# Performance work log

Hardware: AMD Instinct MI355X
Metric: run time of the kernel (lower is better)

The kernel has to match this reference:

```python
import jax, jax.numpy as jnp
import numpy as np

HEADS = 16
DIM_HEAD = 64
SCALE = DIM_HEAD ** -0.5


def setup_inputs() -> dict:
    key = jax.random.key(0)
    ks = jax.random.split(key, 5)
    b, n, dim = 2, 2048, 1024
    inner = HEADS * DIM_HEAD  # 1024
    std = dim ** -0.5
    return {
        "x": jax.random.normal(ks[0], (b, n, dim), jnp.float32),
        "ln_gamma": jnp.ones((dim,), jnp.float32),
        "ln_beta": jnp.zeros((dim,), jnp.float32),
        "W_qk": jax.random.normal(ks[1], (dim, 2 * inner), jnp.float32) * std,
        "W_v": jax.random.normal(ks[2], (dim, inner), jnp.float32) * std,
        "W_out": jax.random.normal(ks[3], (inner, dim), jnp.float32) * std,
        "b_out": jnp.zeros((dim,), jnp.float32),
    }


def _layernorm(x, gamma, beta, eps=1e-5):
    mu = jnp.mean(x, axis=-1, keepdims=True)
    var = jnp.var(x, axis=-1, keepdims=True)
    return (x - mu) * jax.lax.rsqrt(var + eps) * gamma + beta


def reference(x, ln_gamma, ln_beta, W_qk, W_v, W_out, b_out):
    b, n, dim = x.shape
    h, d = HEADS, DIM_HEAD
    xn = _layernorm(x, ln_gamma, ln_beta)
    qk = xn @ W_qk                      # [b, n, 2*h*d]
    q, k = jnp.split(qk, 2, axis=-1)    # each [b, n, h*d]
    v = xn @ W_v                        # [b, n, h*d]
    # b n (h d) -> b h n d
    q = q.reshape(b, n, h, d).transpose(0, 2, 1, 3)
    k = k.reshape(b, n, h, d).transpose(0, 2, 1, 3)
    v = v.reshape(b, n, h, d).transpose(0, 2, 1, 3)
    dots = jnp.einsum('bhid,bhjd->bhij', q, k) * SCALE
    attn = jax.nn.softmax(dots, axis=-1)
    out = jnp.einsum('bhij,bhjd->bhid', attn, v)
    out = out.transpose(0, 2, 1, 3).reshape(b, n, h * d)
    return out @ W_out + b_out
```

## Files before the change

### kernel.cpp

```cpp
#include <hip/hip_runtime.h>

#define HEADS 16
#define DHEAD 64
#define BATCH 2
#define SEQ   2048
#define DIM   1024
#define ROWS  (BATCH*SEQ)
#define SCALE_LOG2E 0.180336880f

typedef short v8s __attribute__((ext_vector_type(8)));
typedef float v4f __attribute__((ext_vector_type(4)));

__device__ __forceinline__ float fast_exp2(float x) {
    return __builtin_amdgcn_exp2f(x);
}

__device__ __forceinline__ unsigned short f2bf(float f) {
    unsigned u = __float_as_uint(f);
    u += 0x7FFFu + ((u >> 16) & 1u);
    return (unsigned short)(u >> 16);
}

__device__ __forceinline__ unsigned pk_bf2(float hi, float lo) {
    return __builtin_amdgcn_perm(__float_as_uint(hi), __float_as_uint(lo), 0x07060302u);
}

#define GLDS16(g, l) __builtin_amdgcn_global_load_lds( \
    (__attribute__((address_space(1))) void*)(g), \
    (__attribute__((address_space(3))) void*)(l), 16, 0, 0)

__global__ __launch_bounds__(256) void ln_kernel(const float* __restrict__ x,
                                                 const float* __restrict__ gamma,
                                                 const float* __restrict__ beta,
                                                 unsigned short* __restrict__ xn) {
    int row = blockIdx.x;
    const float* xr = x + (size_t)row * DIM;
    int t = threadIdx.x;
    float4 v = *(const float4*)(xr + t * 4);
    float s  = v.x + v.y + v.z + v.w;
    float sq = v.x * v.x + v.y * v.y + v.z * v.z + v.w * v.w;
#pragma unroll
    for (int off = 32; off > 0; off >>= 1) {
        s  += __shfl_down(s,  off, 64);
        sq += __shfl_down(sq, off, 64);
    }
    __shared__ float ss[4], ssq[4];
    int wave = t >> 6, lane = t & 63;
    if (lane == 0) { ss[wave] = s; ssq[wave] = sq; }
    __syncthreads();
    float tot  = ss[0] + ss[1] + ss[2] + ss[3];
    float totq = ssq[0] + ssq[1] + ssq[2] + ssq[3];
    float mean = tot * (1.f / DIM);
    float var  = totq * (1.f / DIM) - mean * mean;
    float rstd = rsqrtf(var + 1e-5f);
    float4 g = *(const float4*)(gamma + t * 4);
    float4 bb = *(const float4*)(beta + t * 4);
    ushort4 o;
    o.x = f2bf((v.x - mean) * rstd * g.x + bb.x);
    o.y = f2bf((v.y - mean) * rstd * g.y + bb.y);
    o.z = f2bf((v.z - mean) * rstd * g.z + bb.z);
    o.w = f2bf((v.w - mean) * rstd * g.w + bb.w);
    *(ushort4*)(xn + (size_t)row * DIM + t * 4) = o;
}

__global__ __launch_bounds__(256) void tr_all_kernel(const float* __restrict__ Wqk,
                                                     const float* __restrict__ Wv,
                                                     const float* __restrict__ Wout,
                                                     unsigned short* __restrict__ Tqk,
                                                     unsigned short* __restrict__ Tv,
                                                     unsigned short* __restrict__ To) {
    int z = blockIdx.z;
    const float* W = (z == 0) ? Wqk : (z == 1) ? Wv : Wout;
    unsigned short* Wt = (z == 0) ? Tqk : (z == 1) ? Tv : To;
    int Nw = (z == 0) ? 2048 : 1024;
    int n0 = blockIdx.x * 64, k0 = blockIdx.y * 64;
    if (n0 >= Nw) return;
    __shared__ float tile[64][65];
    int tid = threadIdx.x;
#pragma unroll
    for (int l = 0; l < 4; ++l) {
        int kk = (tid >> 4) + l * 16;
        int nn = (tid & 15) * 4;
        float4 v = *(const float4*)(W + (size_t)(k0 + kk) * Nw + n0 + nn);
        tile[kk][nn + 0] = v.x; tile[kk][nn + 1] = v.y;
        tile[kk][nn + 2] = v.z; tile[kk][nn + 3] = v.w;
    }
    __syncthreads();
#pragma unroll
    for (int l = 0; l < 4; ++l) {
        int cid = tid + l * 256;
        int nn = cid >> 4, kc = (cid & 15) * 4;
        ushort4 o;
        o.x = f2bf(tile[kc + 0][nn]);
        o.y = f2bf(tile[kc + 1][nn]);
        o.z = f2bf(tile[kc + 2][nn]);
        o.w = f2bf(tile[kc + 3][nn]);
        *(ushort4*)(Wt + (size_t)(n0 + nn) * DIM + k0 + kc) = o;
    }
}

template<int BN, bool SWAP>
__device__ __forceinline__ void mm_core2(const unsigned short* __restrict__ A,
                                         const unsigned short* __restrict__ Bt,
                                         int K, int aTile, int bTile,
                                         unsigned short (*As)[32],
                                         unsigned short (*Bs)[32],
                                         v4f (*acc)[4]) {
    constexpr int MI = (BN == 128) ? 4 : 2;
    int t = threadIdx.x;
    int w = t >> 6, L = t & 63, l15 = L & 15, quad = L >> 4;
    int aOff = (BN == 128) ? (w >> 1) * 64 : w * 32;
    int bOff = (BN == 128) ? (w & 1) * 64 : 0;
    int srow = L >> 2, schunk = (L & 3) * 8;
    for (int k0 = 0; k0 < K; k0 += 32) {
        __syncthreads();
#pragma unroll
        for (int j = 0; j < 2; ++j) {
            int g = w * 2 + j;
            GLDS16(A + (size_t)(aTile + g * 16 + srow) * K + k0 + schunk,
                   &As[g * 16][0]);
        }
#pragma unroll
        for (int j = 0; j < BN / 64; ++j) {
            int g = (BN == 128) ? (w * 2 + j) : w;
            GLDS16(Bt + (size_t)(bTile + g * 16 + srow) * K + k0 + schunk,
                   &Bs[g * 16][0]);
        }
        __syncthreads();
        v8s a[MI], b[4];
#pragma unroll
        for (int i = 0; i < MI; ++i) a[i] = *(const v8s*)&As[aOff + i * 16 + l15][quad * 8];
#pragma unroll
        for (int j = 0; j < 4; ++j) b[j] = *(const v8s*)&Bs[bOff + j * 16 + l15][quad * 8];
#pragma unroll
        for (int i = 0; i < MI; ++i)
#pragma unroll
            for (int j = 0; j < 4; ++j)
                acc[i][j] = SWAP
                    ? __builtin_amdgcn_mfma_f32_16x16x32_bf16(b[j], a[i], acc[i][j], 0, 0, 0)
                    : __builtin_amdgcn_mfma_f32_16x16x32_bf16(a[i], b[j], acc[i][j], 0, 0, 0);
    }
}

__global__ __launch_bounds__(256) void gemm_qkv_kernel(const unsigned short* __restrict__ A,
                                                       const unsigned short* __restrict__ Bt,
                                                       unsigned short* __restrict__ q_h,
                                                       unsigned short* __restrict__ k_h,
                                                       unsigned short* __restrict__ v_t) {
    __shared__ __align__(16) unsigned short As[128][32];
    __shared__ __align__(16) unsigned short Bs[128][32];
    int t = threadIdx.x, w = t >> 6, L = t & 63, l15 = L & 15, quad = L >> 4;
    int aTile = blockIdx.y * 128, bTile = blockIdx.x * 128;
    int aOff = (w >> 1) * 64, bOff = (w & 1) * 64;
    v4f acc[4][4] = {};
    if (bTile < 2048) {
        mm_core2<128, true>(A, Bt, DIM, aTile, bTile, As, Bs, acc);
        float sc = (bTile < 1024) ? SCALE_LOG2E : 1.0f;
#pragma unroll
        for (int j = 0; j < 4; ++j) {
            int col = bTile + bOff + j * 16 + quad * 4;
            unsigned short* dst = (col < 1024) ? q_h : k_h;
            int c = col & 1023;
            int h = c >> 6, d = c & 63;
#pragma unroll
            for (int i = 0; i < 4; ++i) {
                int m = aTile + aOff + i * 16 + l15;
                int b = m >> 11, seq = m & 2047;
                ushort4 o;
                o.x = f2bf(acc[i][j][0] * sc); o.y = f2bf(acc[i][j][1] * sc);
                o.z = f2bf(acc[i][j][2] * sc); o.w = f2bf(acc[i][j][3] * sc);
                *(ushort4*)(dst + (((size_t)(b * 16 + h)) * SEQ + seq) * 64 + d) = o;
            }
        }
    } else {
        mm_core2<128, false>(A, Bt, DIM, aTile, bTile, As, Bs, acc);
#pragma unroll
        for (int j = 0; j < 4; ++j) {
            int c = bTile + bOff + j * 16 + l15 - 2048;
            int h = c >> 6, d = c & 63;
#pragma unroll
            for (int i = 0; i < 4; ++i) {
                int m0 = aTile + aOff + i * 16 + quad * 4;
                int b = m0 >> 11, seq0 = m0 & 2047;
                ushort4 o;
                o.x = f2bf(acc[i][j][0]); o.y = f2bf(acc[i][j][1]);
                o.z = f2bf(acc[i][j][2]); o.w = f2bf(acc[i][j][3]);
                *(ushort4*)(v_t + (((size_t)(b * 16 + h)) * 64 + d) * SEQ + seq0) = o;
            }
        }
    }
}

__global__ __launch_bounds__(256) void gemm_out_kernel(const unsigned short* __restrict__ A,
                                                       const unsigned short* __restrict__ Bt,
                                                       const float* __restrict__ bias,
                                                       float* __restrict__ C) {
    __shared__ __align__(16) unsigned short As[128][32];
    __shared__ __align__(16) unsigned short Bs[64][32];
    int t = threadIdx.x, w = t >> 6, L = t & 63, l15 = L & 15, quad = L >> 4;
    int aTile = blockIdx.y * 128, bTile = blockIdx.x * 64;
    v4f acc[2][4] = {};
    mm_core2<64, true>(A, Bt, DIM, aTile, bTile, As, Bs, acc);
#pragma unroll
    for (int j = 0; j < 4; ++j) {
        int n = bTile + j * 16 + quad * 4;
        float4 bv = *(const float4*)(bias + n);
#pragma unroll
        for (int i = 0; i < 2; ++i) {
            int m = aTile + w * 32 + i * 16 + l15;
            float4 o = make_float4(acc[i][j][0] + bv.x, acc[i][j][1] + bv.y,
                                   acc[i][j][2] + bv.z, acc[i][j][3] + bv.w);
            *(float4*)(C + (size_t)m * DIM + n) = o;
        }
    }
}

__global__ __launch_bounds__(256) void attn_kernel(const unsigned short* __restrict__ q_h,
                                                   const unsigned short* __restrict__ k_h,
                                                   const unsigned short* __restrict__ v_t,
                                                   unsigned short* __restrict__ ao) {
    __shared__ __align__(16) unsigned short KF[2][8 * 64 * 8];
    __shared__ __align__(16) unsigned short VF[2][8 * 64 * 8];
    __shared__ __align__(16) unsigned short Pld[4][2][16 * 72];
    int bid = blockIdx.x;
    int wg = (bid & 7) * 64 + (bid >> 3);
    int qt = wg & 15, h = (wg >> 4) & 15, b = wg >> 8;
    int bh = b * HEADS + h;
    int w = threadIdx.x >> 6;
    int L = threadIdx.x & 63, l15 = L & 15, quad = L >> 4;

    const unsigned short* qp = q_h + ((size_t)bh * SEQ + qt * 128 + w * 32 + l15) * 64 + quad * 8;
    v8s qf[2][2];
    qf[0][0] = *(const v8s*)(qp);
    qf[0][1] = *(const v8s*)(qp + 32);
    qf[1][0] = *(const v8s*)(qp + 16 * 64);
    qf[1][1] = *(const v8s*)(qp + 16 * 64 + 32);

    const unsigned short* ksrc = k_h + ((size_t)bh * SEQ + w * 16 + l15) * 64 + quad * 8;
    const unsigned short* vsrc = v_t + ((size_t)bh * 64 + w * 16 + l15) * SEQ + quad * 8;

    GLDS16(ksrc,      &KF[0][(w * 2 + 0) * 512]);
    GLDS16(ksrc + 32, &KF[0][(w * 2 + 1) * 512]);
    GLDS16(vsrc,      &VF[0][(w * 2 + 0) * 512]);
    GLDS16(vsrc + 32, &VF[0][(w * 2 + 1) * 512]);

    v4f o[2][4] = {};
    v4f lacc[2] = {};
    const short ob = (short)0x3F80;
    const v8s ones = {ob, ob, ob, ob, ob, ob, ob, ob};

    int cur = 0;
    for (int j0 = 0; j0 < SEQ; j0 += 64) {
        __syncthreads();
        if (j0 + 64 < SEQ) {
            const unsigned short* kn = ksrc + (size_t)(j0 + 64) * 64;
            const unsigned short* vn = vsrc + (j0 + 64);
            GLDS16(kn,      &KF[cur ^ 1][(w * 2 + 0) * 512]);
            GLDS16(kn + 32, &KF[cur ^ 1][(w * 2 + 1) * 512]);
            GLDS16(vn,      &VF[cur ^ 1][(w * 2 + 0) * 512]);
            GLDS16(vn + 32, &VF[cur ^ 1][(w * 2 + 1) * 512]);
        }
        v8s kf[4][2], vf[4][2];
#pragma unroll
        for (int jt = 0; jt < 4; ++jt) {
            kf[jt][0] = *(const v8s*)&KF[cur][((jt * 2 + 0) * 64 + L) * 8];
            kf[jt][1] = *(const v8s*)&KF[cur][((jt * 2 + 1) * 64 + L) * 8];
            vf[jt][0] = *(const v8s*)&VF[cur][((jt * 2 + 0) * 64 + L) * 8];
            vf[jt][1] = *(const v8s*)&VF[cur][((jt * 2 + 1) * 64 + L) * 8];
        }
        v4f s[2][4] = {};
        __builtin_amdgcn_s_setprio(1);
#pragma unroll
        for (int m = 0; m < 2; ++m)
#pragma unroll
            for (int jt = 0; jt < 4; ++jt) {
                s[m][jt] = __builtin_amdgcn_mfma_f32_16x16x32_bf16(kf[jt][0], qf[m][0], s[m][jt], 0, 0, 0);
                s[m][jt] = __builtin_amdgcn_mfma_f32_16x16x32_bf16(kf[jt][1], qf[m][1], s[m][jt], 0, 0, 0);
            }
        __builtin_amdgcn_s_setprio(0);
#pragma unroll
        for (int m = 0; m < 2; ++m)
#pragma unroll
            for (int jt = 0; jt < 4; ++jt) {
                float p0 = fast_exp2(s[m][jt][0]);
                float p1 = fast_exp2(s[m][jt][1]);
                float p2 = fast_exp2(s[m][jt][2]);
                float p3 = fast_exp2(s[m][jt][3]);
                uint2 pk;
                pk.x = pk_bf2(p1, p0);
                pk.y = pk_bf2(p3, p2);
                *(uint2*)&Pld[w][m][l15 * 72 + jt * 16 + quad * 4] = pk;
            }
#pragma unroll
        for (int m = 0; m < 2; ++m) {
            v8s pb0 = *(const v8s*)&Pld[w][m][l15 * 72 + quad * 8];
            v8s pb1 = *(const v8s*)&Pld[w][m][l15 * 72 + 32 + quad * 8];
            __builtin_amdgcn_s_setprio(1);
#pragma unroll
            for (int dt = 0; dt < 4; ++dt) {
                o[m][dt] = __builtin_amdgcn_mfma_f32_16x16x32_bf16(vf[dt][0], pb0, o[m][dt], 0, 0, 0);
                o[m][dt] = __builtin_amdgcn_mfma_f32_16x16x32_bf16(vf[dt][1], pb1, o[m][dt], 0, 0, 0);
            }
            lacc[m] = __builtin_amdgcn_mfma_f32_16x16x32_bf16(ones, pb0, lacc[m], 0, 0, 0);
            lacc[m] = __builtin_amdgcn_mfma_f32_16x16x32_bf16(ones, pb1, lacc[m], 0, 0, 0);
            __builtin_amdgcn_s_setprio(0);
        }
        cur ^= 1;
    }
#pragma unroll
    for (int m = 0; m < 2; ++m) {
        float inv = 1.f / lacc[m][0];
        int rowg = b * SEQ + qt * 128 + w * 32 + m * 16 + l15;
#pragma unroll
        for (int dt = 0; dt < 4; ++dt) {
            ushort4 ov;
            ov.x = f2bf(o[m][dt][0] * inv);
            ov.y = f2bf(o[m][dt][1] * inv);
            ov.z = f2bf(o[m][dt][2] * inv);
            ov.w = f2bf(o[m][dt][3] * inv);
            *(ushort4*)(ao + (size_t)rowg * DIM + h * 64 + dt * 16 + quad * 4) = ov;
        }
    }
}

extern "C" void kernel_launch(void* const* d_in, const int* in_sizes, int n_in,
                              void* d_out, int out_size, void* d_ws, size_t ws_size,
                              hipStream_t stream) {
    const float* x     = (const float*)d_in[0];
    const float* gamma = (const float*)d_in[1];
    const float* beta  = (const float*)d_in[2];
    const float* Wqk   = (const float*)d_in[3];
    const float* Wv    = (const float*)d_in[4];
    const float* Wout  = (const float*)d_in[5];
    const float* bout  = (const float*)d_in[6];
    float* out = (float*)d_out;

    unsigned short* ws = (unsigned short*)d_ws;
    unsigned short* xn    = ws;
    unsigned short* Wt_qk = xn + (size_t)ROWS * DIM;
    unsigned short* Wt_v  = Wt_qk + (size_t)2048 * DIM;
    unsigned short* Wt_o  = Wt_v + (size_t)DIM * DIM;
    unsigned short* q_h   = Wt_o + (size_t)DIM * DIM;
    unsigned short* k_h   = q_h + (size_t)ROWS * DIM;
    unsigned short* v_t   = k_h + (size_t)ROWS * DIM;
    unsigned short* ao    = v_t + (size_t)ROWS * DIM;

    ln_kernel<<<ROWS, 256, 0, stream>>>(x, gamma, beta, xn);
    tr_all_kernel<<<dim3(32, 16, 3), 256, 0, stream>>>(Wqk, Wv, Wout, Wt_qk, Wt_v, Wt_o);
    gemm_qkv_kernel<<<dim3(3072 / 128, ROWS / 128), 256, 0, stream>>>(xn, Wt_qk, q_h, k_h, v_t);
    attn_kernel<<<dim3(SEQ / 128 * HEADS * BATCH), 256, 0, stream>>>(q_h, k_h, v_t, ao);
    gemm_out_kernel<<<dim3(DIM / 64, ROWS / 128), 256, 0, stream>>>(ao, Wt_o, bout, out);
}
```

Before: 197.4 us.

## Use 8 waves per attention block with 16 query rows each

After: 196.2 us. Within noise of the previous version (-0.6%).

```diff
diff --git a/kernel.cpp b/kernel.cpp
--- a/kernel.cpp
+++ b/kernel.cpp
@@ -215,13 +215,13 @@
     }
 }
 
-__global__ __launch_bounds__(256) void attn_kernel(const unsigned short* __restrict__ q_h,
-                                                   const unsigned short* __restrict__ k_h,
-                                                   const unsigned short* __restrict__ v_t,
-                                                   unsigned short* __restrict__ ao) {
+__global__ __launch_bounds__(512, 4) void attn_kernel(const unsigned short* __restrict__ q_h,
+                                                      const unsigned short* __restrict__ k_h,
+                                                      const unsigned short* __restrict__ v_t,
+                                                      unsigned short* __restrict__ ao) {
     __shared__ __align__(16) unsigned short KF[2][8 * 64 * 8];
     __shared__ __align__(16) unsigned short VF[2][8 * 64 * 8];
-    __shared__ __align__(16) unsigned short Pld[4][2][16 * 72];
+    __shared__ __align__(16) unsigned short Pld[8][16 * 72];
     int bid = blockIdx.x;
     int wg = (bid & 7) * 64 + (bid >> 3);
     int qt = wg & 15, h = (wg >> 4) & 15, b = wg >> 8;
@@ -229,23 +229,18 @@
     int w = threadIdx.x >> 6;
     int L = threadIdx.x & 63, l15 = L & 15, quad = L >> 4;
 
-    const unsigned short* qp = q_h + ((size_t)bh * SEQ + qt * 128 + w * 32 + l15) * 64 + quad * 8;
-    v8s qf[2][2];
-    qf[0][0] = *(const v8s*)(qp);
-    qf[0][1] = *(const v8s*)(qp + 32);
-    qf[1][0] = *(const v8s*)(qp + 16 * 64);
-    qf[1][1] = *(const v8s*)(qp + 16 * 64 + 32);
-
-    const unsigned short* ksrc = k_h + ((size_t)bh * SEQ + w * 16 + l15) * 64 + quad * 8;
-    const unsigned short* vsrc = v_t + ((size_t)bh * 64 + w * 16 + l15) * SEQ + quad * 8;
-
-    GLDS16(ksrc,      &KF[0][(w * 2 + 0) * 512]);
-    GLDS16(ksrc + 32, &KF[0][(w * 2 + 1) * 512]);
-    GLDS16(vsrc,      &VF[0][(w * 2 + 0) * 512]);
-    GLDS16(vsrc + 32, &VF[0][(w * 2 + 1) * 512]);
-
-    v4f o[2][4] = {};
-    v4f lacc[2] = {};
+    const unsigned short* qp = q_h + ((size_t)bh * SEQ + qt * 128 + w * 16 + l15) * 64 + quad * 8;
+    v8s qf0 = *(const v8s*)(qp);
+    v8s qf1 = *(const v8s*)(qp + 32);
+
+    const unsigned short* ksrc = k_h + ((size_t)bh * SEQ + (w >> 1) * 16 + l15) * 64 + (w & 1) * 32 + quad * 8;
+    const unsigned short* vsrc = v_t + ((size_t)bh * 64 + (w >> 1) * 16 + l15) * SEQ + (w & 1) * 32 + quad * 8;
+
+    GLDS16(ksrc, &KF[0][w * 512]);
+    GLDS16(vsrc, &VF[0][w * 512]);
+
+    v4f o[4] = {};
+    v4f lacc = {};
     const short ob = (short)0x3F80;
     const v8s ones = {ob, ob, ob, ob, ob, ob, ob, ob};
 
@@ -253,12 +248,8 @@
     for (int j0 = 0; j0 < SEQ; j0 += 64) {
         __syncthreads();
         if (j0 + 64 < SEQ) {
-            const unsigned short* kn = ksrc + (size_t)(j0 + 64) * 64;
-            const unsigned short* vn = vsrc + (j0 + 64);
-            GLDS16(kn,      &KF[cur ^ 1][(w * 2 + 0) * 512]);
-            GLDS16(kn + 32, &KF[cur ^ 1][(w * 2 + 1) * 512]);
-            GLDS16(vn,      &VF[cur ^ 1][(w * 2 + 0) * 512]);
-            GLDS16(vn + 32, &VF[cur ^ 1][(w * 2 + 1) * 512]);
+            GLDS16(ksrc + (size_t)(j0 + 64) * 64, &KF[cur ^ 1][w * 512]);
+            GLDS16(vsrc + (j0 + 64),              &VF[cur ^ 1][w * 512]);
         }
         v8s kf[4][2], vf[4][2];
 #pragma unroll
@@ -268,58 +259,48 @@
             vf[jt][0] = *(const v8s*)&VF[cur][((jt * 2 + 0) * 64 + L) * 8];
             vf[jt][1] = *(const v8s*)&VF[cur][((jt * 2 + 1) * 64 + L) * 8];
         }
-        v4f s[2][4] = {};
+        v4f s[4] = {};
         __builtin_amdgcn_s_setprio(1);
 #pragma unroll
-        for (int m = 0; m < 2; ++m)
-#pragma unroll
-            for (int jt = 0; jt < 4; ++jt) {
-                s[m][jt] = __builtin_amdgcn_mfma_f32_16x16x32_bf16(kf[jt][0], qf[m][0], s[m][jt], 0, 0, 0);
-                s[m][jt] = __builtin_amdgcn_mfma_f32_16x16x32_bf16(kf[jt][1], qf[m][1], s[m][jt], 0, 0, 0);
-            }
+        for (int jt = 0; jt < 4; ++jt) {
+            s[jt] = __builtin_amdgcn_mfma_f32_16x16x32_bf16(kf[jt][0], qf0, s[jt], 0, 0, 0);
+            s[jt] = __builtin_amdgcn_mfma_f32_16x16x32_bf16(kf[jt][1], qf1, s[jt], 0, 0, 0);
+        }
         __builtin_amdgcn_s_setprio(0);
 #pragma unroll
-        for (int m = 0; m < 2; ++m)
-#pragma unroll
-            for (int jt = 0; jt < 4; ++jt) {
-                float p0 = fast_exp2(s[m][jt][0]);
-                float p1 = fast_exp2(s[m][jt][1]);
-                float p2 = fast_exp2(s[m][jt][2]);
-                float p3 = fast_exp2(s[m][jt][3]);
-                uint2 pk;
-                pk.x = pk_bf2(p1, p0);
-                pk.y = pk_bf2(p3, p2);
-                *(uint2*)&Pld[w][m][l15 * 72 + jt * 16 + quad * 4] = pk;
-            }
-#pragma unroll
-        for (int m = 0; m < 2; ++m) {
-            v8s pb0 = *(const v8s*)&Pld[w][m][l15 * 72 + quad * 8];
-            v8s pb1 = *(const v8s*)&Pld[w][m][l15 * 72 + 32 + quad * 8];
-            __builtin_amdgcn_s_setprio(1);
-#pragma unroll
-            for (int dt = 0; dt < 4; ++dt) {
-                o[m][dt] = __builtin_amdgcn_mfma_f32_16x16x32_bf16(vf[dt][0], pb0, o[m][dt], 0, 0, 0);
-                o[m][dt] = __builtin_amdgcn_mfma_f32_16x16x32_bf16(vf[dt][1], pb1, o[m][dt], 0, 0, 0);
-            }
-            lacc[m] = __builtin_amdgcn_mfma_f32_16x16x32_bf16(ones, pb0, lacc[m], 0, 0, 0);
-            lacc[m] = __builtin_amdgcn_mfma_f32_16x16x32_bf16(ones, pb1, lacc[m], 0, 0, 0);
-            __builtin_amdgcn_s_setprio(0);
-        }
+        for (int jt = 0; jt < 4; ++jt) {
+            float p0 = fast_exp2(s[jt][0]);
+            float p1 = fast_exp2(s[jt][1]);
+            float p2 = fast_exp2(s[jt][2]);
+            float p3 = fast_exp2(s[jt][3]);
+            uint2 pk;
+            pk.x = pk_bf2(p1, p0);
+            pk.y = pk_bf2(p3, p2);
+            *(uint2*)&Pld[w][l15 * 72 + jt * 16 + quad * 4] = pk;
+        }
+        v8s pb0 = *(const v8s*)&Pld[w][l15 * 72 + quad * 8];
+        v8s pb1 = *(const v8s*)&Pld[w][l15 * 72 + 32 + quad * 8];
+        __builtin_amdgcn_s_setprio(1);
+#pragma unroll
+        for (int dt = 0; dt < 4; ++dt) {
+            o[dt] = __builtin_amdgcn_mfma_f32_16x16x32_bf16(vf[dt][0], pb0, o[dt], 0, 0, 0);
+            o[dt] = __builtin_amdgcn_mfma_f32_16x16x32_bf16(vf[dt][1], pb1, o[dt], 0, 0, 0);
+        }
+        lacc = __builtin_amdgcn_mfma_f32_16x16x32_bf16(ones, pb0, lacc, 0, 0, 0);
+        lacc = __builtin_amdgcn_mfma_f32_16x16x32_bf16(ones, pb1, lacc, 0, 0, 0);
+        __builtin_amdgcn_s_setprio(0);
         cur ^= 1;
     }
-#pragma unroll
-    for (int m = 0; m < 2; ++m) {
-        float inv = 1.f / lacc[m][0];
-        int rowg = b * SEQ + qt * 128 + w * 32 + m * 16 + l15;
-#pragma unroll
-        for (int dt = 0; dt < 4; ++dt) {
-            ushort4 ov;
-            ov.x = f2bf(o[m][dt][0] * inv);
-            ov.y = f2bf(o[m][dt][1] * inv);
-            ov.z = f2bf(o[m][dt][2] * inv);
-            ov.w = f2bf(o[m][dt][3] * inv);
-            *(ushort4*)(ao + (size_t)rowg * DIM + h * 64 + dt * 16 + quad * 4) = ov;
-        }
+    float inv = 1.f / lacc[0];
+    int rowg = b * SEQ + qt * 128 + w * 16 + l15;
+#pragma unroll
+    for (int dt = 0; dt < 4; ++dt) {
+        ushort4 ov;
+        ov.x = f2bf(o[dt][0] * inv);
+        ov.y = f2bf(o[dt][1] * inv);
+        ov.z = f2bf(o[dt][2] * inv);
+        ov.w = f2bf(o[dt][3] * inv);
+        *(ushort4*)(ao + (size_t)rowg * DIM + h * 64 + dt * 16 + quad * 4) = ov;
     }
 }
 
@@ -348,6 +329,6 @@
     ln_kernel<<<ROWS, 256, 0, stream>>>(x, gamma, beta, xn);
     tr_all_kernel<<<dim3(32, 16, 3), 256, 0, stream>>>(Wqk, Wv, Wout, Wt_qk, Wt_v, Wt_o);
     gemm_qkv_kernel<<<dim3(3072 / 128, ROWS / 128), 256, 0, stream>>>(xn, Wt_qk, q_h, k_h, v_t);
-    attn_kernel<<<dim3(SEQ / 128 * HEADS * BATCH), 256, 0, stream>>>(q_h, k_h, v_t, ao);
+    attn_kernel<<<dim3(SEQ / 128 * HEADS * BATCH), 512, 0, stream>>>(q_h, k_h, v_t, ao);
     gemm_out_kernel<<<dim3(DIM / 64, ROWS / 128), 256, 0, stream>>>(ao, Wt_o, bout, out);
 }
```

## Load K/V fragments directly from global memory instead of LDS double-buffering

Applied to the files above, without the earlier changes.

Result: slower. 263.2 us (+33.3%).

```diff
diff --git a/kernel.cpp b/kernel.cpp
--- a/kernel.cpp
+++ b/kernel.cpp
@@ -215,12 +215,10 @@
     }
 }
 
-__global__ __launch_bounds__(256) void attn_kernel(const unsigned short* __restrict__ q_h,
-                                                   const unsigned short* __restrict__ k_h,
-                                                   const unsigned short* __restrict__ v_t,
-                                                   unsigned short* __restrict__ ao) {
-    __shared__ __align__(16) unsigned short KF[2][8 * 64 * 8];
-    __shared__ __align__(16) unsigned short VF[2][8 * 64 * 8];
+__global__ __launch_bounds__(256, 2) void attn_kernel(const unsigned short* __restrict__ q_h,
+                                                      const unsigned short* __restrict__ k_h,
+                                                      const unsigned short* __restrict__ v_t,
+                                                      unsigned short* __restrict__ ao) {
     __shared__ __align__(16) unsigned short Pld[4][2][16 * 72];
     int bid = blockIdx.x;
     int wg = (bid & 7) * 64 + (bid >> 3);
@@ -236,37 +234,28 @@
     qf[1][0] = *(const v8s*)(qp + 16 * 64);
     qf[1][1] = *(const v8s*)(qp + 16 * 64 + 32);
 
-    const unsigned short* ksrc = k_h + ((size_t)bh * SEQ + w * 16 + l15) * 64 + quad * 8;
-    const unsigned short* vsrc = v_t + ((size_t)bh * 64 + w * 16 + l15) * SEQ + quad * 8;
-
-    GLDS16(ksrc,      &KF[0][(w * 2 + 0) * 512]);
-    GLDS16(ksrc + 32, &KF[0][(w * 2 + 1) * 512]);
-    GLDS16(vsrc,      &VF[0][(w * 2 + 0) * 512]);
-    GLDS16(vsrc + 32, &VF[0][(w * 2 + 1) * 512]);
+    const unsigned short* kp = k_h + ((size_t)bh * SEQ + l15) * 64 + quad * 8;
+    const unsigned short* vp = v_t + ((size_t)bh * 64 + l15) * SEQ + quad * 8;
 
     v4f o[2][4] = {};
     v4f lacc[2] = {};
     const short ob = (short)0x3F80;
     const v8s ones = {ob, ob, ob, ob, ob, ob, ob, ob};
 
-    int cur = 0;
     for (int j0 = 0; j0 < SEQ; j0 += 64) {
-        __syncthreads();
-        if (j0 + 64 < SEQ) {
-            const unsigned short* kn = ksrc + (size_t)(j0 + 64) * 64;
-            const unsigned short* vn = vsrc + (j0 + 64);
-            GLDS16(kn,      &KF[cur ^ 1][(w * 2 + 0) * 512]);
-            GLDS16(kn + 32, &KF[cur ^ 1][(w * 2 + 1) * 512]);
-            GLDS16(vn,      &VF[cur ^ 1][(w * 2 + 0) * 512]);
-            GLDS16(vn + 32, &VF[cur ^ 1][(w * 2 + 1) * 512]);
-        }
+        if ((j0 & 127) == 0) __syncthreads();
         v8s kf[4][2], vf[4][2];
 #pragma unroll
         for (int jt = 0; jt < 4; ++jt) {
-            kf[jt][0] = *(const v8s*)&KF[cur][((jt * 2 + 0) * 64 + L) * 8];
-            kf[jt][1] = *(const v8s*)&KF[cur][((jt * 2 + 1) * 64 + L) * 8];
-            vf[jt][0] = *(const v8s*)&VF[cur][((jt * 2 + 0) * 64 + L) * 8];
-            vf[jt][1] = *(const v8s*)&VF[cur][((jt * 2 + 1) * 64 + L) * 8];
+            const unsigned short* kr = kp + (size_t)(j0 + jt * 16) * 64;
+            kf[jt][0] = *(const v8s*)(kr);
+            kf[jt][1] = *(const v8s*)(kr + 32);
+        }
+#pragma unroll
+        for (int dt = 0; dt < 4; ++dt) {
+            const unsigned short* vr = vp + (size_t)dt * 16 * SEQ + j0;
+            vf[dt][0] = *(const v8s*)(vr);
+            vf[dt][1] = *(const v8s*)(vr + 32);
         }
         v4f s[2][4] = {};
         __builtin_amdgcn_s_setprio(1);
@@ -305,7 +294,6 @@
             lacc[m] = __builtin_amdgcn_mfma_f32_16x16x32_bf16(ones, pb1, lacc[m], 0, 0, 0);
             __builtin_amdgcn_s_setprio(0);
         }
-        cur ^= 1;
     }
 #pragma unroll
     for (int m = 0; m < 2; ++m) {
```
